# Optimization experiments

Hardware: AMD Instinct MI355X
Metric: run time of the kernel (lower is better)

## Reference

```python
import jax, jax.numpy as jnp
import numpy as np

B, T, ND, DH, DZ = 32, 4096, 32, 128, 128
IN_DIM = 2 * ND + DH  # 192


def setup_inputs() -> dict:
    key = jax.random.key(0)
    ks = jax.random.split(key, 11)
    s = 1.0 / np.sqrt(DZ)  # PyTorch GRUCell init scale
    return {
        "z0": jax.random.normal(ks[0], (B, DZ), jnp.float32),
        # sorted irregular timestamps per series
        "t_dyn": jnp.sort(jax.random.uniform(ks[1], (B, T), jnp.float32) * 100.0, axis=1),
        "Y_dyn": jax.random.normal(ks[2], (B, T, ND), jnp.float32),
        "M_dyn": (jax.random.uniform(ks[3], (B, T, ND)) > 0.5).astype(jnp.float32),
        "dyn_lens": jax.random.randint(ks[4], (B,), 1, T + 1, dtype=jnp.int32),
        "h_path_vals": jax.random.normal(ks[5], (B, T, DH), jnp.float32),
        "W_ih": jax.random.uniform(ks[6], (3 * DZ, IN_DIM), jnp.float32, -s, s),
        "b_ih": jax.random.uniform(ks[7], (3 * DZ,), jnp.float32, -s, s),
        "W_hh": jax.random.uniform(ks[8], (3 * DZ, DZ), jnp.float32, -s, s),
        "b_hh": jax.random.uniform(ks[9], (3 * DZ,), jnp.float32, -s, s),
        "log_gamma": jnp.zeros((DZ,), jnp.float32),
    }


def reference(z0, t_dyn, Y_dyn, M_dyn, dyn_lens, h_path_vals, W_ih, b_ih, W_hh, b_hh, log_gamma):
    gamma = jax.nn.softplus(log_gamma)  # (d_z,)
    Tm = t_dyn.shape[1]
    # concat dynamic features once; precompute all input-side gate projections as one big GEMM
    x = jnp.concatenate([Y_dyn, M_dyn, h_path_vals], axis=-1)        # (B,T,IN_DIM)
    gi_all = jnp.einsum('bti,gi->btg', x, W_ih) + b_ih               # (B,T,3*d_z)
    active = (jnp.arange(Tm)[:, None] < dyn_lens[None, :]).astype(z0.dtype)  # (T,B)

    def step(carry, xs):
        z, t_prev = carry
        t_k, gi, a = xs                 # (B,), (B,3dz), (B,)
        dt = jnp.maximum(t_k - t_prev, 0.0)
        z_d = z * jnp.exp(-gamma * dt[:, None])      # exponential decay
        gh = z_d @ W_hh.T + b_hh
        i_r, i_u, i_n = jnp.split(gi, 3, axis=-1)
        h_r, h_u, h_n = jnp.split(gh, 3, axis=-1)
        r = jax.nn.sigmoid(i_r + h_r)
        u = jax.nn.sigmoid(i_u + h_u)
        n = jnp.tanh(i_n + r * h_n)
        z_new = (1.0 - u) * n + u * z_d
        am = a[:, None]
        z_out = am * z_new + (1.0 - am) * z_d        # length masking
        return (z_out, t_k), z_out

    xs = (t_dyn.T, jnp.swapaxes(gi_all, 0, 1), active)  # time-major
    (z_final, _), Z = jax.lax.scan(step, (z0, t_dyn[:, 0]), xs)
    Z_traj = jnp.swapaxes(Z, 0, 1)                      # (B,T,d_z)
    return z_final, Z_traj
```

## Files before the change

### kernel.cpp

```cpp
#include <hip/hip_runtime.h>
#include <hip/hip_bf16.h>
#include <stdint.h>

typedef unsigned short u16;

#define NB  32
#define NT  4096
#define NDZ 128
#define NG  384
#define NIN 192

__device__ __forceinline__ float rlane(float v, int k) {
  return __int_as_float(__builtin_amdgcn_readlane(__float_as_int(v), k));
}
__device__ __forceinline__ float fast_rcp(float x) { return __builtin_amdgcn_rcpf(x); }
__device__ __forceinline__ float sigmoid_f(float x) { return fast_rcp(1.f + __expf(-x)); }
__device__ __forceinline__ float tanh_f(float x) {
  return 1.f - 2.f * fast_rcp(1.f + __expf(2.f * x));
}
__device__ __forceinline__ u16 f2bf(float f) {
  unsigned u = __float_as_uint(f);
  return (u16)((u + 0x7fffu + ((u >> 16) & 1u)) >> 16);
}
__device__ __forceinline__ float bf2f(u16 u) { return __uint_as_float((unsigned)u << 16); }

__device__ __forceinline__ void bar_lds() {
  asm volatile("s_waitcnt lgkmcnt(0)\n\ts_barrier" ::: "memory");
}

__device__ __forceinline__ float giload(const float* p) { return *p; }
__device__ __forceinline__ float giload(const u16* p)   { return bf2f(*p); }
__device__ __forceinline__ void store8(float* p, const float* v) {
  float4 a = {v[0], v[1], v[2], v[3]}, b = {v[4], v[5], v[6], v[7]};
  *(float4*)p = a; *(float4*)(p + 4) = b;
}
__device__ __forceinline__ void store8(u16* p, const float* v) {
  uint4 o;
  o.x = (unsigned)f2bf(v[0]) | ((unsigned)f2bf(v[1]) << 16);
  o.y = (unsigned)f2bf(v[2]) | ((unsigned)f2bf(v[3]) << 16);
  o.z = (unsigned)f2bf(v[4]) | ((unsigned)f2bf(v[5]) << 16);
  o.w = (unsigned)f2bf(v[6]) | ((unsigned)f2bf(v[7]) << 16);
  *(uint4*)p = o;
}

#define GM 128
#define GN 128
#define LDSS 132

template <typename GT>
__global__ __launch_bounds__(256) void gemm_gi(
    const float* __restrict__ Y, const float* __restrict__ M,
    const float* __restrict__ H, const float* __restrict__ Wih,
    const float* __restrict__ bih, GT* __restrict__ gi)
{
  __shared__ float As[32 * LDSS];
  __shared__ float Bs[32 * LDSS];
  const int tid = threadIdx.x;
  const size_t m0 = (size_t)blockIdx.x * GM;
  const int n0 = blockIdx.y * GN;
  const int tm = tid & 15;
  const int tn = tid >> 4;

  float acc[8][8];
#pragma unroll
  for (int i = 0; i < 8; ++i)
#pragma unroll
    for (int j = 0; j < 8; ++j) acc[i][j] = 0.f;

#pragma unroll
  for (int kc = 0; kc < 6; ++kc) {
    const float* src; int stride; int off;
    if (kc == 0)      { src = Y; stride = 32;  off = 0; }
    else if (kc == 1) { src = M; stride = 32;  off = 0; }
    else              { src = H; stride = 128; off = (kc - 2) * 32; }
#pragma unroll
    for (int it = 0; it < 4; ++it) {
      int x = tid + it * 256;
      int row = x >> 3, q = x & 7;
      float4 v = *(const float4*)(src + (m0 + (size_t)row) * stride + off + q * 4);
      As[(q * 4 + 0) * LDSS + row] = v.x;
      As[(q * 4 + 1) * LDSS + row] = v.y;
      As[(q * 4 + 2) * LDSS + row] = v.z;
      As[(q * 4 + 3) * LDSS + row] = v.w;
    }
#pragma unroll
    for (int it = 0; it < 4; ++it) {
      int x = tid + it * 256;
      int g = x >> 3, q = x & 7;
      float4 v = *(const float4*)(Wih + (size_t)(n0 + g) * NIN + kc * 32 + q * 4);
      Bs[(q * 4 + 0) * LDSS + g] = v.x;
      Bs[(q * 4 + 1) * LDSS + g] = v.y;
      Bs[(q * 4 + 2) * LDSS + g] = v.z;
      Bs[(q * 4 + 3) * LDSS + g] = v.w;
    }
    __syncthreads();
#pragma unroll
    for (int kk = 0; kk < 32; ++kk) {
      float4 a0 = *(const float4*)&As[kk * LDSS + tm * 8];
      float4 a1 = *(const float4*)&As[kk * LDSS + tm * 8 + 4];
      float4 b0 = *(const float4*)&Bs[kk * LDSS + tn * 8];
      float4 b1 = *(const float4*)&Bs[kk * LDSS + tn * 8 + 4];
      float av[8] = {a0.x, a0.y, a0.z, a0.w, a1.x, a1.y, a1.z, a1.w};
      float bv[8] = {b0.x, b0.y, b0.z, b0.w, b1.x, b1.y, b1.z, b1.w};
#pragma unroll
      for (int i = 0; i < 8; ++i)
#pragma unroll
        for (int j = 0; j < 8; ++j)
          acc[i][j] = __builtin_fmaf(av[i], bv[j], acc[i][j]);
    }
    __syncthreads();
  }
  float bv[8];
#pragma unroll
  for (int j = 0; j < 8; ++j) bv[j] = bih[n0 + tn * 8 + j];
#pragma unroll
  for (int i = 0; i < 8; ++i) {
    size_t row = m0 + (size_t)(tm * 8 + i);
    GT* o = gi + row * NG + n0 + tn * 8;
    float v[8];
#pragma unroll
    for (int j = 0; j < 8; ++j) v[j] = acc[i][j] + bv[j];
    store8(o, v);
  }
}

#define KS 16

template <typename GT>
__global__ __launch_bounds__(512, 1) void scan_k(
    const float* __restrict__ zinit, const float* __restrict__ tdyn,
    const int* __restrict__ lens, const float* __restrict__ Whh,
    const float* __restrict__ bhh, const float* __restrict__ lgam,
    const GT* __restrict__ gi, float* __restrict__ out)
{
  const int b = blockIdx.x;
  const int tid = threadIdx.x;
  const int lane = tid & 63;
  const int w = tid >> 6;
  const int k0 = w * KS;
  const int e = lane & 15;
  const int j = k0 + e;

  __shared__ float P0[8][NG];
  __shared__ float P1[8][NG];

  float2 wp[3][KS];
#pragma unroll
  for (int p = 0; p < 3; ++p) {
    const float4* r0 = (const float4*)(Whh + (size_t)(lane + 128 * p) * NDZ + k0);
    const float4* r1 = (const float4*)(Whh + (size_t)(lane + 128 * p + 64) * NDZ + k0);
#pragma unroll
    for (int q = 0; q < 4; ++q) {
      float4 v0 = r0[q];
      float4 v1 = r1[q];
      wp[p][4 * q + 0].x = v0.x; wp[p][4 * q + 0].y = v1.x;
      wp[p][4 * q + 1].x = v0.y; wp[p][4 * q + 1].y = v1.y;
      wp[p][4 * q + 2].x = v0.z; wp[p][4 * q + 2].y = v1.z;
      wp[p][4 * q + 3].x = v0.w; wp[p][4 * q + 3].y = v1.w;
    }
  }

  const int len = lens[b];
  const float* tp = tdyn + (size_t)b * NT;
  const GT* gb = gi + (size_t)b * NT * NG;
  float* traj = out + (size_t)NB * NDZ + (size_t)b * NT * NDZ;

  float zc = zinit[b * NDZ + j];
  const float lg = lgam[j];
  const float gam = (lg > 15.f) ? lg : __logf(1.f + __expf(lg));
  const float br = bhh[j], bu = bhh[NDZ + j], bn = bhh[2 * NDZ + j];
  float t_prev = tp[0];
  float zdr = zc;

  const int gsel = lane >> 4;
  const int g3 = (gsel < 3) ? gsel : 0;
  const int prow = j + 128 * g3;

  float ptkA = tp[1];
  float ptkB = tp[2];
  float pgrA = giload(gb + j), pguA = giload(gb + NDZ + j), pgnA = giload(gb + 2 * NDZ + j);
  float pgrB = giload(gb + NG + j), pguB = giload(gb + NG + NDZ + j), pgnB = giload(gb + NG + 2 * NDZ + j);

  auto stepf = [&](float (*PB)[NG], float& ptkX, float& pgrX, float& pguX, float& pgnX, int t) {
    const bool active = (t < len);
    if (active) {
      float2 a0 = {0.f, 0.f}, a1 = {0.f, 0.f}, a2 = {0.f, 0.f};
#pragma unroll
      for (int k = 0; k < KS; ++k) {
        const float zk = rlane(zdr, k);
        a0.x = __builtin_fmaf(wp[0][k].x, zk, a0.x);
        a0.y = __builtin_fmaf(wp[0][k].y, zk, a0.y);
        a1.x = __builtin_fmaf(wp[1][k].x, zk, a1.x);
        a1.y = __builtin_fmaf(wp[1][k].y, zk, a1.y);
        a2.x = __builtin_fmaf(wp[2][k].x, zk, a2.x);
        a2.y = __builtin_fmaf(wp[2][k].y, zk, a2.y);
      }
      PB[w][lane]       = a0.x;  PB[w][lane + 64]  = a0.y;
      PB[w][lane + 128] = a1.x;  PB[w][lane + 192] = a1.y;
      PB[w][lane + 256] = a2.x;  PB[w][lane + 320] = a2.y;
    }
    bar_lds();

    const float zd = zdr;
    if (active) {
      float s0 = PB[0][prow] + PB[1][prow];
      float s1 = PB[2][prow] + PB[3][prow];
      float s2 = PB[4][prow] + PB[5][prow];
      float s3 = PB[6][prow] + PB[7][prow];
      const float sg = (s0 + s1) + (s2 + s3);
      const float su = __shfl(sg, e + 16, 64);
      const float sn = __shfl(sg, e + 32, 64);
      const float r = sigmoid_f(sg + br + pgrX);
      const float u = sigmoid_f(su + bu + pguX);
      const float n = tanh_f(__builtin_fmaf(r, sn + bn, pgnX));
      zc = (1.f - u) * n + u * zd;
    } else {
      zc = zd;
    }
    if (lane < 16) traj[(size_t)t * NDZ + j] = zc;

    const float tk = ptkX;
    const float dt = fmaxf(tk - t_prev, 0.f);
    zdr = zc * __expf(-gam * dt);
    t_prev = tk;

    const int t2 = (t + 2 < NT) ? (t + 2) : (NT - 1);
    const int t3 = (t + 3 < NT) ? (t + 3) : (NT - 1);
    ptkX = tp[t3];
    const GT* g2 = gb + (size_t)t2 * NG;
    pgrX = giload(g2 + j);
    pguX = giload(g2 + NDZ + j);
    pgnX = giload(g2 + 2 * NDZ + j);
  };

  for (int t = 0; t < NT; t += 2) {
    stepf(P0, ptkA, pgrA, pguA, pgnA, t);
    stepf(P1, ptkB, pgrB, pguB, pgnB, t + 1);
  }
  if (lane < 16) out[b * NDZ + j] = zc;
}

extern "C" void kernel_launch(void* const* d_in, const int* in_sizes, int n_in,
                              void* d_out, int out_size, void* d_ws, size_t ws_size,
                              hipStream_t stream) {
  const float* z0   = (const float*)d_in[0];
  const float* tdyn = (const float*)d_in[1];
  const float* Y    = (const float*)d_in[2];
  const float* M    = (const float*)d_in[3];
  const int*   lens = (const int*)d_in[4];
  const float* H    = (const float*)d_in[5];
  const float* Wih  = (const float*)d_in[6];
  const float* bih  = (const float*)d_in[7];
  const float* Whh  = (const float*)d_in[8];
  const float* bhh  = (const float*)d_in[9];
  const float* lgam = (const float*)d_in[10];
  float* out = (float*)d_out;

  const size_t needF32 = (size_t)NB * NT * NG * sizeof(float);
  dim3 ggrid((NB * NT) / GM, NG / GN);
  if (ws_size >= needF32) {
    float* gi = (float*)d_ws;
    gemm_gi<float><<<ggrid, 256, 0, stream>>>(Y, M, H, Wih, bih, gi);
    scan_k<float><<<dim3(NB), 512, 0, stream>>>(z0, tdyn, lens, Whh, bhh, lgam, gi, out);
  } else {
    u16* gi = (u16*)d_ws;
    gemm_gi<u16><<<ggrid, 256, 0, stream>>>(Y, M, H, Wih, bih, gi);
    scan_k<u16><<<dim3(NB), 512, 0, stream>>>(z0, tdyn, lens, Whh, bhh, lgam, gi, out);
  }
}
```

Measured before the change: 3.480 ms.

## Batch 16 sequences per block and compute recurrent matvec with bf16 MFMA

Replaces the per-batch scalar FMA scan (one block per sequence, readlane broadcasts plus LDS partial-sum reduction) with a block that processes 16 sequences together. W_hh is held in registers as bf16 MFMA fragments, and each step stages the decayed state in LDS as bf16 before issuing 16x16x32 MFMAs. This removes the cross-wave reduction and shuffles, but cuts the grid to 2 blocks and rounds the hidden state and weights to bf16 in the recurrence, which can compound error over 4096 steps.

```diff
diff --git a/kernel.cpp b/kernel.cpp
--- a/kernel.cpp
+++ b/kernel.cpp
@@ -10,9 +10,6 @@
 #define NG  384
 #define NIN 192
 
-__device__ __forceinline__ float rlane(float v, int k) {
-  return __int_as_float(__builtin_amdgcn_readlane(__float_as_int(v), k));
-}
 __device__ __forceinline__ float fast_rcp(float x) { return __builtin_amdgcn_rcpf(x); }
 __device__ __forceinline__ float sigmoid_f(float x) { return fast_rcp(1.f + __expf(-x)); }
 __device__ __forceinline__ float tanh_f(float x) {
@@ -22,14 +19,11 @@
   unsigned u = __float_as_uint(f);
   return (u16)((u + 0x7fffu + ((u >> 16) & 1u)) >> 16);
 }
-__device__ __forceinline__ float bf2f(u16 u) { return __uint_as_float((unsigned)u << 16); }
 
 __device__ __forceinline__ void bar_lds() {
   asm volatile("s_waitcnt lgkmcnt(0)\n\ts_barrier" ::: "memory");
 }
 
-__device__ __forceinline__ float giload(const float* p) { return *p; }
-__device__ __forceinline__ float giload(const u16* p)   { return bf2f(*p); }
 __device__ __forceinline__ void store8(float* p, const float* v) {
   float4 a = {v[0], v[1], v[2], v[3]}, b = {v[4], v[5], v[6], v[7]};
   *(float4*)p = a; *(float4*)(p + 4) = b;
@@ -124,120 +118,143 @@
   }
 }
 
-#define KS 16
+#define BPB  16
+#define KPAD 136
+
+typedef __attribute__((ext_vector_type(8))) __bf16 bfrag;
+typedef __attribute__((ext_vector_type(4))) float ffrag;
+
+template <typename GT> struct Raw;
+template <> struct Raw<u16>   { using T = uint2;  };
+template <> struct Raw<float> { using T = float4; };
+
+__device__ __forceinline__ void unpk(const uint2& u, float* v) {
+  v[0] = __uint_as_float(u.x << 16);
+  v[1] = __uint_as_float(u.x & 0xffff0000u);
+  v[2] = __uint_as_float(u.y << 16);
+  v[3] = __uint_as_float(u.y & 0xffff0000u);
+}
+__device__ __forceinline__ void unpk(const float4& f, float* v) {
+  v[0] = f.x; v[1] = f.y; v[2] = f.z; v[3] = f.w;
+}
 
 template <typename GT>
-__global__ __launch_bounds__(512, 1) void scan_k(
+__global__ __launch_bounds__(512, 2) void scan_m(
     const float* __restrict__ zinit, const float* __restrict__ tdyn,
     const int* __restrict__ lens, const float* __restrict__ Whh,
     const float* __restrict__ bhh, const float* __restrict__ lgam,
     const GT* __restrict__ gi, float* __restrict__ out)
 {
-  const int b = blockIdx.x;
-  const int tid = threadIdx.x;
+  const int tid  = threadIdx.x;
   const int lane = tid & 63;
-  const int w = tid >> 6;
-  const int k0 = w * KS;
-  const int e = lane & 15;
-  const int j = k0 + e;
-
-  __shared__ float P0[8][NG];
-  __shared__ float P1[8][NG];
-
-  float2 wp[3][KS];
-#pragma unroll
-  for (int p = 0; p < 3; ++p) {
-    const float4* r0 = (const float4*)(Whh + (size_t)(lane + 128 * p) * NDZ + k0);
-    const float4* r1 = (const float4*)(Whh + (size_t)(lane + 128 * p + 64) * NDZ + k0);
-#pragma unroll
-    for (int q = 0; q < 4; ++q) {
-      float4 v0 = r0[q];
-      float4 v1 = r1[q];
-      wp[p][4 * q + 0].x = v0.x; wp[p][4 * q + 0].y = v1.x;
-      wp[p][4 * q + 1].x = v0.y; wp[p][4 * q + 1].y = v1.y;
-      wp[p][4 * q + 2].x = v0.z; wp[p][4 * q + 2].y = v1.z;
-      wp[p][4 * q + 3].x = v0.w; wp[p][4 * q + 3].y = v1.w;
-    }
-  }
-
-  const int len = lens[b];
-  const float* tp = tdyn + (size_t)b * NT;
-  const GT* gb = gi + (size_t)b * NT * NG;
-  float* traj = out + (size_t)NB * NDZ + (size_t)b * NT * NDZ;
-
-  float zc = zinit[b * NDZ + j];
-  const float lg = lgam[j];
-  const float gam = (lg > 15.f) ? lg : __logf(1.f + __expf(lg));
-  const float br = bhh[j], bu = bhh[NDZ + j], bn = bhh[2 * NDZ + j];
+  const int w    = tid >> 6;
+  const int q    = lane >> 4;
+  const int bl   = lane & 15;
+  const int batch = blockIdx.x * BPB + bl;
+  const int j0   = 16 * w + 4 * q;
+
+  __shared__ __align__(16) u16 ZL0[BPB * KPAD];
+  __shared__ __align__(16) u16 ZL1[BPB * KPAD];
+
+  union BU { bfrag v; u16 s[8]; };
+  bfrag afr0[4], afr1[4], afr2[4];
+#pragma unroll
+  for (int g = 0; g < 3; ++g) {
+    const float* wr = Whh + (size_t)(g * NDZ + 16 * w + bl) * NDZ;
+#pragma unroll
+    for (int kk = 0; kk < 4; ++kk) {
+      float4 v0 = *(const float4*)(wr + 32 * kk + 8 * q);
+      float4 v1 = *(const float4*)(wr + 32 * kk + 8 * q + 4);
+      BU u;
+      u.s[0] = f2bf(v0.x); u.s[1] = f2bf(v0.y); u.s[2] = f2bf(v0.z); u.s[3] = f2bf(v0.w);
+      u.s[4] = f2bf(v1.x); u.s[5] = f2bf(v1.y); u.s[6] = f2bf(v1.z); u.s[7] = f2bf(v1.w);
+      if (g == 0) afr0[kk] = u.v;
+      else if (g == 1) afr1[kk] = u.v;
+      else afr2[kk] = u.v;
+    }
+  }
+
+  const int len = lens[batch];
+  const float* tp = tdyn + (size_t)batch * NT;
+  const GT* gl = gi + ((size_t)batch * NT) * NG + j0;
+  float* traj = out + (size_t)NB * NDZ + (size_t)batch * NT * NDZ;
+
+  float zc[4], gam[4], bg0[4], bg1[4], bg2[4];
+  {
+    float4 z4 = *(const float4*)(zinit + batch * NDZ + j0);
+    zc[0] = z4.x; zc[1] = z4.y; zc[2] = z4.z; zc[3] = z4.w;
+    float4 l4 = *(const float4*)(lgam + j0);
+    float lgv[4] = {l4.x, l4.y, l4.z, l4.w};
+#pragma unroll
+    for (int r = 0; r < 4; ++r)
+      gam[r] = (lgv[r] > 15.f) ? lgv[r] : __logf(1.f + __expf(lgv[r]));
+    float4 b0 = *(const float4*)(bhh + j0);
+    float4 b1 = *(const float4*)(bhh + NDZ + j0);
+    float4 b2 = *(const float4*)(bhh + 2 * NDZ + j0);
+    bg0[0] = b0.x; bg0[1] = b0.y; bg0[2] = b0.z; bg0[3] = b0.w;
+    bg1[0] = b1.x; bg1[1] = b1.y; bg1[2] = b1.z; bg1[3] = b1.w;
+    bg2[0] = b2.x; bg2[1] = b2.y; bg2[2] = b2.z; bg2[3] = b2.w;
+  }
   float t_prev = tp[0];
-  float zdr = zc;
-
-  const int gsel = lane >> 4;
-  const int g3 = (gsel < 3) ? gsel : 0;
-  const int prow = j + 128 * g3;
-
-  float ptkA = tp[1];
-  float ptkB = tp[2];
-  float pgrA = giload(gb + j), pguA = giload(gb + NDZ + j), pgnA = giload(gb + 2 * NDZ + j);
-  float pgrB = giload(gb + NG + j), pguB = giload(gb + NG + NDZ + j), pgnB = giload(gb + NG + 2 * NDZ + j);
-
-  auto stepf = [&](float (*PB)[NG], float& ptkX, float& pgrX, float& pguX, float& pgnX, int t) {
-    const bool active = (t < len);
-    if (active) {
-      float2 a0 = {0.f, 0.f}, a1 = {0.f, 0.f}, a2 = {0.f, 0.f};
-#pragma unroll
-      for (int k = 0; k < KS; ++k) {
-        const float zk = rlane(zdr, k);
-        a0.x = __builtin_fmaf(wp[0][k].x, zk, a0.x);
-        a0.y = __builtin_fmaf(wp[0][k].y, zk, a0.y);
-        a1.x = __builtin_fmaf(wp[1][k].x, zk, a1.x);
-        a1.y = __builtin_fmaf(wp[1][k].y, zk, a1.y);
-        a2.x = __builtin_fmaf(wp[2][k].x, zk, a2.x);
-        a2.y = __builtin_fmaf(wp[2][k].y, zk, a2.y);
-      }
-      PB[w][lane]       = a0.x;  PB[w][lane + 64]  = a0.y;
-      PB[w][lane + 128] = a1.x;  PB[w][lane + 192] = a1.y;
-      PB[w][lane + 256] = a2.x;  PB[w][lane + 320] = a2.y;
-    }
+
+  using RT = typename Raw<GT>::T;
+  float ptkA = tp[0], ptkB = tp[1];
+  RT prA0 = *(const RT*)(gl);
+  RT prA1 = *(const RT*)(gl + NDZ);
+  RT prA2 = *(const RT*)(gl + 2 * NDZ);
+  RT prB0 = *(const RT*)(gl + NG);
+  RT prB1 = *(const RT*)(gl + NG + NDZ);
+  RT prB2 = *(const RT*)(gl + NG + 2 * NDZ);
+
+  auto stepf = [&](u16* ZB, float& ptkX, RT& px0, RT& px1, RT& px2, int t) {
+    const float tk = ptkX;
+    const float dtv = fmaxf(tk - t_prev, 0.f);
+    t_prev = tk;
+    float zd[4];
+#pragma unroll
+    for (int r = 0; r < 4; ++r) zd[r] = zc[r] * __expf(-gam[r] * dtv);
+    unsigned p0 = (unsigned)f2bf(zd[0]) | ((unsigned)f2bf(zd[1]) << 16);
+    unsigned p1 = (unsigned)f2bf(zd[2]) | ((unsigned)f2bf(zd[3]) << 16);
+    *(uint2*)&ZB[bl * KPAD + j0] = uint2{p0, p1};
     bar_lds();
 
-    const float zd = zdr;
-    if (active) {
-      float s0 = PB[0][prow] + PB[1][prow];
-      float s1 = PB[2][prow] + PB[3][prow];
-      float s2 = PB[4][prow] + PB[5][prow];
-      float s3 = PB[6][prow] + PB[7][prow];
-      const float sg = (s0 + s1) + (s2 + s3);
-      const float su = __shfl(sg, e + 16, 64);
-      const float sn = __shfl(sg, e + 32, 64);
-      const float r = sigmoid_f(sg + br + pgrX);
-      const float u = sigmoid_f(su + bu + pguX);
-      const float n = tanh_f(__builtin_fmaf(r, sn + bn, pgnX));
-      zc = (1.f - u) * n + u * zd;
-    } else {
-      zc = zd;
-    }
-    if (lane < 16) traj[(size_t)t * NDZ + j] = zc;
-
-    const float tk = ptkX;
-    const float dt = fmaxf(tk - t_prev, 0.f);
-    zdr = zc * __expf(-gam * dt);
-    t_prev = tk;
+    ffrag acc0 = {0.f, 0.f, 0.f, 0.f}, acc1 = acc0, acc2 = acc0;
+#pragma unroll
+    for (int kk = 0; kk < 4; ++kk) {
+      bfrag bf = *(const bfrag*)&ZB[bl * KPAD + 32 * kk + 8 * q];
+      acc0 = __builtin_amdgcn_mfma_f32_16x16x32_bf16(afr0[kk], bf, acc0, 0, 0, 0);
+      acc1 = __builtin_amdgcn_mfma_f32_16x16x32_bf16(afr1[kk], bf, acc1, 0, 0, 0);
+      acc2 = __builtin_amdgcn_mfma_f32_16x16x32_bf16(afr2[kk], bf, acc2, 0, 0, 0);
+    }
+
+    float gr[4], gu[4], gn[4];
+    unpk(px0, gr); unpk(px1, gu); unpk(px2, gn);
+    const bool act = (t < len);
+    float zo[4];
+#pragma unroll
+    for (int r = 0; r < 4; ++r) {
+      const float rr = sigmoid_f(acc0[r] + bg0[r] + gr[r]);
+      const float uu = sigmoid_f(acc1[r] + bg1[r] + gu[r]);
+      const float nn = tanh_f(__builtin_fmaf(rr, acc2[r] + bg2[r], gn[r]));
+      const float zn = (1.f - uu) * nn + uu * zd[r];
+      zo[r] = act ? zn : zd[r];
+      zc[r] = zo[r];
+    }
+    *(float4*)(traj + (size_t)t * NDZ + j0) = float4{zo[0], zo[1], zo[2], zo[3]};
 
     const int t2 = (t + 2 < NT) ? (t + 2) : (NT - 1);
-    const int t3 = (t + 3 < NT) ? (t + 3) : (NT - 1);
-    ptkX = tp[t3];
-    const GT* g2 = gb + (size_t)t2 * NG;
-    pgrX = giload(g2 + j);
-    pguX = giload(g2 + NDZ + j);
-    pgnX = giload(g2 + 2 * NDZ + j);
+    ptkX = tp[t2];
+    const GT* g2 = gl + (size_t)t2 * NG;
+    px0 = *(const RT*)(g2);
+    px1 = *(const RT*)(g2 + NDZ);
+    px2 = *(const RT*)(g2 + 2 * NDZ);
   };
 
   for (int t = 0; t < NT; t += 2) {
-    stepf(P0, ptkA, pgrA, pguA, pgnA, t);
-    stepf(P1, ptkB, pgrB, pguB, pgnB, t + 1);
-  }
-  if (lane < 16) out[b * NDZ + j] = zc;
+    stepf(ZL0, ptkA, prA0, prA1, prA2, t);
+    stepf(ZL1, ptkB, prB0, prB1, prB2, t + 1);
+  }
+  *(float4*)(out + batch * NDZ + j0) = float4{zc[0], zc[1], zc[2], zc[3]};
 }
 
 extern "C" void kernel_launch(void* const* d_in, const int* in_sizes, int n_in,
@@ -261,10 +278,10 @@
   if (ws_size >= needF32) {
     float* gi = (float*)d_ws;
     gemm_gi<float><<<ggrid, 256, 0, stream>>>(Y, M, H, Wih, bih, gi);
-    scan_k<float><<<dim3(NB), 512, 0, stream>>>(z0, tdyn, lens, Whh, bhh, lgam, gi, out);
+    scan_m<float><<<dim3(NB / BPB), 512, 0, stream>>>(z0, tdyn, lens, Whh, bhh, lgam, gi, out);
   } else {
     u16* gi = (u16*)d_ws;
     gemm_gi<u16><<<ggrid, 256, 0, stream>>>(Y, M, H, Wih, bih, gi);
-    scan_k<u16><<<dim3(NB), 512, 0, stream>>>(z0, tdyn, lens, Whh, bhh, lgam, gi, out);
-  }
-}
+    scan_m<u16><<<dim3(NB / BPB), 512, 0, stream>>>(z0, tdyn, lens, Whh, bhh, lgam, gi, out);
+  }
+}
```

After: 10.26 ms. 2.95x slower.

## Restructure GRU scan to one thread per hidden unit with fp16 dot2

Applied to the files above, without the earlier changes.

The recurrent scan kernel now uses 128 threads per batch instead of 512. Each thread owns one hidden unit and holds its three W_hh rows in registers as packed fp16. The decayed state is broadcast through LDS as fp16, and each thread computes its full 128-long dot products with v_dot2 instructions. This removes the cross-wave partial-sum reduction, the shuffles and the second LDS pass per step. The cost is lower precision in the recurrent matmul, a large register footprint of 192 packed registers, and only two waves per block, which leaves less latency hiding.

```diff
diff --git a/kernel.cpp b/kernel.cpp
--- a/kernel.cpp
+++ b/kernel.cpp
@@ -3,6 +3,7 @@
 #include <stdint.h>
 
 typedef unsigned short u16;
+typedef __fp16 h2 __attribute__((ext_vector_type(2)));
 
 #define NB  32
 #define NT  4096
@@ -10,9 +11,12 @@
 #define NG  384
 #define NIN 192
 
-__device__ __forceinline__ float rlane(float v, int k) {
-  return __int_as_float(__builtin_amdgcn_readlane(__float_as_int(v), k));
-}
+#if defined(__has_builtin)
+#if __has_builtin(__builtin_amdgcn_fdot2)
+#define HAS_FDOT2 1
+#endif
+#endif
+
 __device__ __forceinline__ float fast_rcp(float x) { return __builtin_amdgcn_rcpf(x); }
 __device__ __forceinline__ float sigmoid_f(float x) { return fast_rcp(1.f + __expf(-x)); }
 __device__ __forceinline__ float tanh_f(float x) {
@@ -23,6 +27,18 @@
   return (u16)((u + 0x7fffu + ((u >> 16) & 1u)) >> 16);
 }
 __device__ __forceinline__ float bf2f(u16 u) { return __uint_as_float((unsigned)u << 16); }
+__device__ __forceinline__ u16 f2h16(float f) {
+  __fp16 h = (__fp16)f;
+  return __builtin_bit_cast(u16, h);
+}
+__device__ __forceinline__ float fdot2f(h2 a, h2 b, float c) {
+#ifdef HAS_FDOT2
+  return __builtin_amdgcn_fdot2(a, b, c, false);
+#else
+  return __builtin_fmaf((float)a.x, (float)b.x,
+         __builtin_fmaf((float)a.y, (float)b.y, c));
+#endif
+}
 
 __device__ __forceinline__ void bar_lds() {
   asm volatile("s_waitcnt lgkmcnt(0)\n\ts_barrier" ::: "memory");
@@ -124,39 +140,51 @@
   }
 }
 
-#define KS 16
+#define DOT4(QW, M0)                                                          \
+  { h2 zk0 = __builtin_bit_cast(h2, (QW).x);                                  \
+    ar0 = fdot2f(wr_[(M0) + 0], zk0, ar0);                                    \
+    au0 = fdot2f(wu_[(M0) + 0], zk0, au0);                                    \
+    an0 = fdot2f(wn_[(M0) + 0], zk0, an0);                                    \
+    h2 zk1 = __builtin_bit_cast(h2, (QW).y);                                  \
+    ar1 = fdot2f(wr_[(M0) + 1], zk1, ar1);                                    \
+    au1 = fdot2f(wu_[(M0) + 1], zk1, au1);                                    \
+    an1 = fdot2f(wn_[(M0) + 1], zk1, an1);                                    \
+    h2 zk2 = __builtin_bit_cast(h2, (QW).z);                                  \
+    ar2 = fdot2f(wr_[(M0) + 2], zk2, ar2);                                    \
+    au2 = fdot2f(wu_[(M0) + 2], zk2, au2);                                    \
+    an2 = fdot2f(wn_[(M0) + 2], zk2, an2);                                    \
+    h2 zk3 = __builtin_bit_cast(h2, (QW).w);                                  \
+    ar3 = fdot2f(wr_[(M0) + 3], zk3, ar3);                                    \
+    au3 = fdot2f(wu_[(M0) + 3], zk3, au3);                                    \
+    an3 = fdot2f(wn_[(M0) + 3], zk3, an3); }
 
 template <typename GT>
-__global__ __launch_bounds__(512, 1) void scan_k(
+__global__ __launch_bounds__(128, 1) void scan_p(
     const float* __restrict__ zinit, const float* __restrict__ tdyn,
     const int* __restrict__ lens, const float* __restrict__ Whh,
     const float* __restrict__ bhh, const float* __restrict__ lgam,
     const GT* __restrict__ gi, float* __restrict__ out)
 {
   const int b = blockIdx.x;
-  const int tid = threadIdx.x;
-  const int lane = tid & 63;
-  const int w = tid >> 6;
-  const int k0 = w * KS;
-  const int e = lane & 15;
-  const int j = k0 + e;
-
-  __shared__ float P0[8][NG];
-  __shared__ float P1[8][NG];
-
-  float2 wp[3][KS];
-#pragma unroll
-  for (int p = 0; p < 3; ++p) {
-    const float4* r0 = (const float4*)(Whh + (size_t)(lane + 128 * p) * NDZ + k0);
-    const float4* r1 = (const float4*)(Whh + (size_t)(lane + 128 * p + 64) * NDZ + k0);
-#pragma unroll
-    for (int q = 0; q < 4; ++q) {
-      float4 v0 = r0[q];
-      float4 v1 = r1[q];
-      wp[p][4 * q + 0].x = v0.x; wp[p][4 * q + 0].y = v1.x;
-      wp[p][4 * q + 1].x = v0.y; wp[p][4 * q + 1].y = v1.y;
-      wp[p][4 * q + 2].x = v0.z; wp[p][4 * q + 2].y = v1.z;
-      wp[p][4 * q + 3].x = v0.w; wp[p][4 * q + 3].y = v1.w;
+  const int j = threadIdx.x;
+
+  __shared__ __align__(16) u16 Z0[NDZ];
+  __shared__ __align__(16) u16 Z1[NDZ];
+
+  h2 wr_[64], wu_[64], wn_[64];
+  {
+    const float4* pr = (const float4*)(Whh + (size_t)j * NDZ);
+    const float4* pu = (const float4*)(Whh + (size_t)(j + NDZ) * NDZ);
+    const float4* pn = (const float4*)(Whh + (size_t)(j + 2 * NDZ) * NDZ);
+#pragma unroll
+    for (int q = 0; q < 32; ++q) {
+      float4 vr = pr[q], vu = pu[q], vn = pn[q];
+      wr_[2 * q]     = __builtin_amdgcn_cvt_pkrtz(vr.x, vr.y);
+      wr_[2 * q + 1] = __builtin_amdgcn_cvt_pkrtz(vr.z, vr.w);
+      wu_[2 * q]     = __builtin_amdgcn_cvt_pkrtz(vu.x, vu.y);
+      wu_[2 * q + 1] = __builtin_amdgcn_cvt_pkrtz(vu.z, vu.w);
+      wn_[2 * q]     = __builtin_amdgcn_cvt_pkrtz(vn.x, vn.y);
+      wn_[2 * q + 1] = __builtin_amdgcn_cvt_pkrtz(vn.z, vn.w);
     }
   }
 
@@ -172,57 +200,48 @@
   float t_prev = tp[0];
   float zdr = zc;
 
-  const int gsel = lane >> 4;
-  const int g3 = (gsel < 3) ? gsel : 0;
-  const int prow = j + 128 * g3;
-
   float ptkA = tp[1];
   float ptkB = tp[2];
   float pgrA = giload(gb + j), pguA = giload(gb + NDZ + j), pgnA = giload(gb + 2 * NDZ + j);
   float pgrB = giload(gb + NG + j), pguB = giload(gb + NG + NDZ + j), pgnB = giload(gb + NG + 2 * NDZ + j);
 
-  auto stepf = [&](float (*PB)[NG], float& ptkX, float& pgrX, float& pguX, float& pgnX, int t) {
+  auto stepf = [&](u16* ZB, float& ptkX, float& pgrX, float& pguX, float& pgnX, int t) {
+    const float tk = ptkX;
+    const float ef = __expf(-gam * fmaxf(tk - t_prev, 0.f));
+    t_prev = tk;
+    const float crX = br + pgrX;
+    const float cuX = bu + pguX;
+
+    const float zd = zdr;
     const bool active = (t < len);
     if (active) {
-      float2 a0 = {0.f, 0.f}, a1 = {0.f, 0.f}, a2 = {0.f, 0.f};
-#pragma unroll
-      for (int k = 0; k < KS; ++k) {
-        const float zk = rlane(zdr, k);
-        a0.x = __builtin_fmaf(wp[0][k].x, zk, a0.x);
-        a0.y = __builtin_fmaf(wp[0][k].y, zk, a0.y);
-        a1.x = __builtin_fmaf(wp[1][k].x, zk, a1.x);
-        a1.y = __builtin_fmaf(wp[1][k].y, zk, a1.y);
-        a2.x = __builtin_fmaf(wp[2][k].x, zk, a2.x);
-        a2.y = __builtin_fmaf(wp[2][k].y, zk, a2.y);
+      ZB[j] = f2h16(zd);
+    }
+    bar_lds();
+
+    if (active) {
+      float ar0 = 0.f, ar1 = 0.f, ar2 = 0.f, ar3 = 0.f;
+      float au0 = 0.f, au1 = 0.f, au2 = 0.f, au3 = 0.f;
+      float an0 = 0.f, an1 = 0.f, an2 = 0.f, an3 = 0.f;
+      const uint4* zr = (const uint4*)ZB;
+#pragma unroll
+      for (int rr = 0; rr < 16; ++rr) {
+        uint4 qv = zr[rr];
+        DOT4(qv, rr * 4);
       }
-      PB[w][lane]       = a0.x;  PB[w][lane + 64]  = a0.y;
-      PB[w][lane + 128] = a1.x;  PB[w][lane + 192] = a1.y;
-      PB[w][lane + 256] = a2.x;  PB[w][lane + 320] = a2.y;
-    }
-    bar_lds();
-
-    const float zd = zdr;
-    if (active) {
-      float s0 = PB[0][prow] + PB[1][prow];
-      float s1 = PB[2][prow] + PB[3][prow];
-      float s2 = PB[4][prow] + PB[5][prow];
-      float s3 = PB[6][prow] + PB[7][prow];
-      const float sg = (s0 + s1) + (s2 + s3);
-      const float su = __shfl(sg, e + 16, 64);
-      const float sn = __shfl(sg, e + 32, 64);
-      const float r = sigmoid_f(sg + br + pgrX);
-      const float u = sigmoid_f(su + bu + pguX);
+      const float sr = (ar0 + ar1) + (ar2 + ar3);
+      const float su = (au0 + au1) + (au2 + au3);
+      const float sn = (an0 + an1) + (an2 + an3);
+      const float r = sigmoid_f(sr + crX);
+      const float u = sigmoid_f(su + cuX);
       const float n = tanh_f(__builtin_fmaf(r, sn + bn, pgnX));
-      zc = (1.f - u) * n + u * zd;
+      zc = __builtin_fmaf(u, zd - n, n);
     } else {
       zc = zd;
     }
-    if (lane < 16) traj[(size_t)t * NDZ + j] = zc;
-
-    const float tk = ptkX;
-    const float dt = fmaxf(tk - t_prev, 0.f);
-    zdr = zc * __expf(-gam * dt);
-    t_prev = tk;
+    traj[(size_t)t * NDZ + j] = zc;
+
+    zdr = zc * ef;
 
     const int t2 = (t + 2 < NT) ? (t + 2) : (NT - 1);
     const int t3 = (t + 3 < NT) ? (t + 3) : (NT - 1);
@@ -234,10 +253,10 @@
   };
 
   for (int t = 0; t < NT; t += 2) {
-    stepf(P0, ptkA, pgrA, pguA, pgnA, t);
-    stepf(P1, ptkB, pgrB, pguB, pgnB, t + 1);
-  }
-  if (lane < 16) out[b * NDZ + j] = zc;
+    stepf(Z0, ptkA, pgrA, pguA, pgnA, t);
+    stepf(Z1, ptkB, pgrB, pguB, pgnB, t + 1);
+  }
+  out[b * NDZ + j] = zc;
 }
 
 extern "C" void kernel_launch(void* const* d_in, const int* in_sizes, int n_in,
@@ -261,10 +280,10 @@
   if (ws_size >= needF32) {
     float* gi = (float*)d_ws;
     gemm_gi<float><<<ggrid, 256, 0, stream>>>(Y, M, H, Wih, bih, gi);
-    scan_k<float><<<dim3(NB), 512, 0, stream>>>(z0, tdyn, lens, Whh, bhh, lgam, gi, out);
+    scan_p<float><<<dim3(NB), 128, 0, stream>>>(z0, tdyn, lens, Whh, bhh, lgam, gi, out);
   } else {
     u16* gi = (u16*)d_ws;
     gemm_gi<u16><<<ggrid, 256, 0, stream>>>(Y, M, H, Wih, bih, gi);
-    scan_k<u16><<<dim3(NB), 512, 0, stream>>>(z0, tdyn, lens, Whh, bhh, lgam, gi, out);
-  }
-}
+    scan_p<u16><<<dim3(NB), 128, 0, stream>>>(z0, tdyn, lens, Whh, bhh, lgam, gi, out);
+  }
+}
```

Result: faster. 2.999 ms (-13.8%).
